# Optimization experiments

Measured on AMD Instinct MI355X. Metric: run time of the kernel, lower is better.

Reference implementation:

```python
import jax, jax.numpy as jnp
import numpy as np

SCALE_FACTORS = (0.5, 1.0)
ITERATIONS = (2, 2)
TAU = (1.0, 1.0)
SIGMA = (1.0, 1.0)
SIGMA_CUTOFF = 3.0
EPS = 1e-9
DHW = ('NCDHW', 'OIDHW', 'NCDHW')


def gaussian_kernel1d(sigma):
    radius = int(round(sigma * SIGMA_CUTOFF))
    x = np.arange(-radius, radius + 1, dtype=np.float32)
    k = np.exp(-0.5 * (x / sigma) ** 2)
    return jnp.asarray(k / k.sum())


def smooth3d(vf, kernel):
    # separable depthwise Gaussian over the 3 spatial axes; vf: (B,C,D,H,W)
    C = vf.shape[1]
    n = kernel.shape[0]
    for axis in range(3):
        shape = [1, 1, 1]
        shape[axis] = n
        kern = jnp.broadcast_to(kernel.reshape(1, 1, *shape), (C, 1, *shape))
        vf = jax.lax.conv_general_dilated(vf, kern, (1, 1, 1), 'SAME',
                                          feature_group_count=C, dimension_numbers=DHW)
    return vf


def resize_tri(x, spatial):
    return jax.image.resize(x, x.shape[:2] + tuple(spatial), method='trilinear')


def warp(img, flow):
    # trilinear grid-sample with voxel-space displacement, border clamping
    B, C, D, H, W = img.shape
    gz, gy, gx = jnp.meshgrid(jnp.arange(D, dtype=img.dtype),
                              jnp.arange(H, dtype=img.dtype),
                              jnp.arange(W, dtype=img.dtype), indexing='ij')
    base = jnp.stack([gz, gy, gx])  # (3,D,H,W)

    def one(im, fl):
        z = jnp.clip(base[0] + fl[0], 0.0, D - 1)
        y = jnp.clip(base[1] + fl[1], 0.0, H - 1)
        x = jnp.clip(base[2] + fl[2], 0.0, W - 1)
        z0 = jnp.floor(z); y0 = jnp.floor(y); x0 = jnp.floor(x)
        wz = z - z0; wy = y - y0; wx = x - x0
        z0i = z0.astype(jnp.int32); y0i = y0.astype(jnp.int32); x0i = x0.astype(jnp.int32)
        z1i = jnp.minimum(z0i + 1, D - 1)
        y1i = jnp.minimum(y0i + 1, H - 1)
        x1i = jnp.minimum(x0i + 1, W - 1)

        def g(zi, yi, xi):
            return im[:, zi, yi, xi]  # (C,D,H,W)

        return (g(z0i, y0i, x0i) * (1 - wz) * (1 - wy) * (1 - wx)
                + g(z0i, y0i, x1i) * (1 - wz) * (1 - wy) * wx
                + g(z0i, y1i, x0i) * (1 - wz) * wy * (1 - wx)
                + g(z0i, y1i, x1i) * (1 - wz) * wy * wx
                + g(z1i, y0i, x0i) * wz * (1 - wy) * (1 - wx)
                + g(z1i, y0i, x1i) * wz * (1 - wy) * wx
                + g(z1i, y1i, x0i) * wz * wy * (1 - wx)
                + g(z1i, y1i, x1i) * wz * wy * wx)

    return jax.vmap(one)(img, flow)


def demon_forces(warped, fixed):
    # 'active' demon forces: gradient of the warped moving image
    diff = warped - fixed                                  # (B,1,D,H,W)
    g = jnp.stack(jnp.gradient(warped[:, 0], axis=(1, 2, 3)), axis=1)  # (B,3,D,H,W)
    denom = jnp.sum(g * g, axis=1, keepdims=True) + diff * diff + EPS
    return diff * g / denom


def conv3(x, w, b=None):
    y = jax.lax.conv_general_dilated(x, w, (1, 1, 1), 'SAME', dimension_numbers=DHW)
    return y if b is None else y + b.reshape(1, -1, 1, 1, 1)


def inorm(x):  # InstanceNorm3d, affine=False, eps=1e-5
    m = x.mean(axis=(2, 3, 4), keepdims=True)
    v = x.var(axis=(2, 3, 4), keepdims=True)
    return (x - m) * jax.lax.rsqrt(v + 1e-5)


def mish(x):
    return x * jnp.tanh(jax.nn.softplus(x))


def updater(x, w1, w2, w3, w4, b4):
    x = mish(inorm(conv3(x, w1)))
    x = mish(inorm(conv3(x, w2)))
    x = mish(inorm(conv3(x, w3)))
    return conv3(x, w4, b4)


def match_vf(vf, spatial):
    old = vf.shape[2:]
    if tuple(old) == tuple(spatial):
        return vf
    vf2 = resize_tri(vf, spatial)
    scale = jnp.array([s1 / s2 for s1, s2 in zip(spatial, old)], dtype=vf.dtype)
    return vf2 * scale.reshape(1, 3, 1, 1, 1)


def registration(image, moving, w1, w2, w3, w4, b4):
    vf = None
    for i, (sf, iters) in enumerate(zip(SCALE_FACTORS, ITERATIONS)):
        spatial = tuple(int(s * sf) for s in image.shape[2:])
        si = resize_tri(image, spatial)
        smov = resize_tri(moving, spatial)
        vf = jnp.zeros((image.shape[0], 3) + spatial, image.dtype) if vf is None else match_vf(vf, spatial)
        kernel = gaussian_kernel1d(SIGMA[i]).astype(image.dtype)
        for _ in range(iters):
            warped = warp(smov, vf)
            forces = demon_forces(warped, si)
            feat = jnp.concatenate([forces, si, warped], axis=1)  # 5 channels
            vf = vf + TAU[i] * updater(feat, w1, w2, w3, w4, b4)
            vf = smooth3d(vf, kernel)
    vf = match_vf(vf, image.shape[2:])
    warped_full = warp(moving, vf)
    return warped_full, vf


def setup_inputs() -> dict:
    key = jax.random.key(0)
    ks = jax.random.split(key, 8)
    D = H = W = 96
    return {
        'image': jax.random.uniform(ks[0], (1, 1, D, H, W), jnp.float32),
        'mask': jnp.ones((1, 1, D, H, W), jnp.float32),
        'moving': jax.random.uniform(ks[1], (1, 1, D, H, W), jnp.float32),
        'spacing': jnp.ones((3,), jnp.float32),
        'w1': jax.random.normal(ks[2], (32, 5, 3, 3, 3), jnp.float32) * 0.05,
        'w2': jax.random.normal(ks[3], (64, 32, 3, 3, 3), jnp.float32) * 0.05,
        'w3': jax.random.normal(ks[4], (32, 64, 3, 3, 3), jnp.float32) * 0.05,
        'w4': jax.random.normal(ks[5], (3, 32, 3, 3, 3), jnp.float32) * 0.05,
        'b4': jnp.zeros((3,), jnp.float32),
    }


def reference(image, mask, moving, spacing, w1, w2, w3, w4, b4):
    # mask only feeds metrics/early-stopping (disabled: early_stopping_fn='none');
    # spacing unused since use_image_spacing=False.
    return registration(image, moving, w1, w2, w3, w4, b4)
```

## Files before the change

### kernel.cpp

```cpp
#include <hip/hip_runtime.h>
#include <hip/hip_bf16.h>


#define DEV __device__ __forceinline__
typedef __hip_bfloat16 bf16;
typedef __attribute__((ext_vector_type(8))) short short8;
typedef __attribute__((ext_vector_type(4))) float f32x4;

DEV float bfu(unsigned int u) {
  union { unsigned int i; float f; } x; x.i = u << 16; return x.f;
}
DEV unsigned short fbf(float f) {
  __hip_bfloat16 h = __float2bfloat16(f);
  return __builtin_bit_cast(unsigned short, h);
}

DEV float mishf(float v) {
  if (v > 20.f) return v;
  float u = __expf(v);
  float w = u * (u + 2.f);
  return v * (w / (w + 2.f));
}

__global__ void zero_k(float* __restrict__ p, int n) {
  int i = blockIdx.x * 256 + threadIdx.x;
  if (i < n) p[i] = 0.f;
}
__global__ void copy_k(const float* __restrict__ in, float* __restrict__ out, int n) {
  int i = blockIdx.x * 256 + threadIdx.x;
  if (i < n) out[i] = in[i];
}

__global__ void pack_wf_k(const float* __restrict__ w, bf16* __restrict__ dst,
                          int NWT, int KB, int COR, int CIR) {
  int idx = blockIdx.x * 256 + threadIdx.x;
  int tot = 27 * NWT * KB * 512;
  if (idx >= tot) return;
  int j = idx & 7;
  int lane = (idx >> 3) & 63;
  int frag = idx >> 9;
  int kb = frag % KB;
  int r2 = frag / KB;
  int nwt = r2 % NWT;
  int off = r2 / NWT;
  int co = nwt * 16 + (lane & 15);
  int ci = (kb * 4 + (lane >> 4)) * 8 + j;
  float v = (co < COR && ci < CIR) ? w[((size_t)co * CIR + ci) * 27 + off] : 0.f;
  dst[idx] = __float2bfloat16(v);
}

__global__ void pack_w1p_k(const float* __restrict__ w, bf16* __restrict__ dst) {
  int idx = blockIdx.x * 256 + threadIdx.x;
  if (idx >= 7 * 2 * 512) return;
  int j = idx & 7;
  int lane = (idx >> 3) & 63;
  int frag = idx >> 9;
  int nw = frag & 1;
  int rd = frag >> 1;
  int co = nw * 16 + (lane & 15);
  int tap = rd * 4 + (lane >> 4);
  float v = (tap < 27 && j < 5) ? w[((size_t)co * 5 + j) * 27 + tap] : 0.f;
  dst[idx] = __float2bfloat16(v);
}

DEV int ds_taps(int i, int n_out, int* j0, float* w) {
  if (i == 0) { *j0 = 0; w[0] = 3.f/7.f; w[1] = 3.f/7.f; w[2] = 1.f/7.f; return 3; }
  if (i == n_out - 1) { *j0 = 2*i - 1; w[0] = 1.f/7.f; w[1] = 3.f/7.f; w[2] = 3.f/7.f; return 3; }
  *j0 = 2*i - 1; w[0] = 0.125f; w[1] = 0.375f; w[2] = 0.375f; w[3] = 0.125f; return 4;
}
DEV void up_taps(int i, int n_in, int* j0, int* j1, float* w0, float* w1) {
  if (i & 1) {
    int k = i >> 1;
    if (k + 1 >= n_in) { *j0 = n_in - 1; *j1 = n_in - 1; *w0 = 1.f; *w1 = 0.f; }
    else { *j0 = k; *j1 = k + 1; *w0 = 0.75f; *w1 = 0.25f; }
  } else {
    int k = i >> 1;
    if (k == 0) { *j0 = 0; *j1 = 0; *w0 = 1.f; *w1 = 0.f; }
    else { *j0 = k - 1; *j1 = k; *w0 = 0.25f; *w1 = 0.75f; }
  }
}

__global__ void down2x_k(const float* __restrict__ in, float* __restrict__ out,
                         int Do, int Ho, int Wo) {
  const int Hi = 2 * Ho, Wi = 2 * Wo;
  const int No = Do * Ho * Wo;
  int i = blockIdx.x * 256 + threadIdx.x;
  if (i >= No) return;
  int xo = i % Wo; int t = i / Wo; int yo = t % Ho; int zo = t / Ho;
  int jz0, jy0, jx0; float wz[4], wy[4], wx[4];
  int cz = ds_taps(zo, Do, &jz0, wz);
  int cy = ds_taps(yo, Ho, &jy0, wy);
  int cx = ds_taps(xo, Wo, &jx0, wx);
  float s = 0.f;
  for (int a = 0; a < cz; ++a) {
    const float* pz = in + (size_t)(jz0 + a) * Hi * Wi;
    for (int b = 0; b < cy; ++b) {
      const float* py = pz + (size_t)(jy0 + b) * Wi;
      float wab = wz[a] * wy[b];
      for (int d = 0; d < cx; ++d) s += wab * wx[d] * py[jx0 + d];
    }
  }
  out[i] = s;
}

__global__ void up2x_vf_k(const float* __restrict__ in, float* __restrict__ out,
                          int Do, int Ho, int Wo) {
  const int Di = Do / 2, Hi = Ho / 2, Wi = Wo / 2;
  const int No = Do * Ho * Wo;
  const int c = blockIdx.y;
  int i = blockIdx.x * 256 + threadIdx.x;
  if (i >= No) return;
  int xo = i % Wo; int t = i / Wo; int yo = t % Ho; int zo = t / Ho;
  int jz0, jz1, jy0, jy1, jx0, jx1; float wz0, wz1, wy0, wy1, wx0, wx1;
  up_taps(zo, Di, &jz0, &jz1, &wz0, &wz1);
  up_taps(yo, Hi, &jy0, &jy1, &wy0, &wy1);
  up_taps(xo, Wi, &jx0, &jx1, &wx0, &wx1);
  const float* p = in + (size_t)c * Di * Hi * Wi;
  float v00 = wx0 * p[(jz0 * Hi + jy0) * Wi + jx0] + wx1 * p[(jz0 * Hi + jy0) * Wi + jx1];
  float v01 = wx0 * p[(jz0 * Hi + jy1) * Wi + jx0] + wx1 * p[(jz0 * Hi + jy1) * Wi + jx1];
  float v10 = wx0 * p[(jz1 * Hi + jy0) * Wi + jx0] + wx1 * p[(jz1 * Hi + jy0) * Wi + jx1];
  float v11 = wx0 * p[(jz1 * Hi + jy1) * Wi + jx0] + wx1 * p[(jz1 * Hi + jy1) * Wi + jx1];
  float s = wz0 * (wy0 * v00 + wy1 * v01) + wz1 * (wy0 * v10 + wy1 * v11);
  out[(size_t)c * No + i] = 2.f * s;
}

DEV float warp1(const float* __restrict__ img, const float* __restrict__ vf,
                int x, int y, int z, size_t i, int D, int H, int W, size_t N) {
  float zc = fminf(fmaxf((float)z + vf[i], 0.f), (float)(D - 1));
  float yc = fminf(fmaxf((float)y + vf[N + i], 0.f), (float)(H - 1));
  float xc = fminf(fmaxf((float)x + vf[2 * N + i], 0.f), (float)(W - 1));
  float zf = floorf(zc), yf = floorf(yc), xf = floorf(xc);
  int z0 = (int)zf, y0 = (int)yf, x0 = (int)xf;
  float wz = zc - zf, wy = yc - yf, wx = xc - xf;
  int z1 = min(z0 + 1, D - 1), y1 = min(y0 + 1, H - 1), x1 = min(x0 + 1, W - 1);
  const int HW = H * W;
  float v000 = img[z0 * HW + y0 * W + x0];
  float v001 = img[z0 * HW + y0 * W + x1];
  float v010 = img[z0 * HW + y1 * W + x0];
  float v011 = img[z0 * HW + y1 * W + x1];
  float v100 = img[z1 * HW + y0 * W + x0];
  float v101 = img[z1 * HW + y0 * W + x1];
  float v110 = img[z1 * HW + y1 * W + x0];
  float v111 = img[z1 * HW + y1 * W + x1];
  return v000 * (1 - wz) * (1 - wy) * (1 - wx)
       + v001 * (1 - wz) * (1 - wy) * wx
       + v010 * (1 - wz) * wy * (1 - wx)
       + v011 * (1 - wz) * wy * wx
       + v100 * wz * (1 - wy) * (1 - wx)
       + v101 * wz * (1 - wy) * wx
       + v110 * wz * wy * (1 - wx)
       + v111 * wz * wy * wx;
}

__global__ void warp_k(const float* __restrict__ img, const float* __restrict__ vf,
                       float* __restrict__ out, int D, int H, int W) {
  const size_t N = (size_t)D * H * W;
  size_t i = (size_t)blockIdx.x * 256 + threadIdx.x;
  if (i >= N) return;
  int x = i % W; int t = i / W; int y = t % H; int z = t / H;
  out[i] = warp1(img, vf, x, y, z, i, D, H, W, N);
}

__global__ void __launch_bounds__(256) warpforce_k(
    const float* __restrict__ img, const float* __restrict__ vf,
    const float* __restrict__ si, bf16* __restrict__ feat, int D, int H, int W) {
  __shared__ float wt[600];
  const size_t N = (size_t)D * H * W;
  const int t = threadIdx.x;
  const int tx = t & 7, ty = (t >> 3) & 7, tz = t >> 6;
  const int gx0 = blockIdx.x * 8, gy0 = blockIdx.y * 8, gz0 = blockIdx.z * 4;
  for (int cid = t; cid < 600; cid += 256) {
    int hx = cid % 10; int r = cid / 10; int hy = r % 10; int hz = r / 10;
    int gz = gz0 + hz - 1, gy = gy0 + hy - 1, gx = gx0 + hx - 1;
    float w = 0.f;
    if (((unsigned)gz < (unsigned)D) & ((unsigned)gy < (unsigned)H) & ((unsigned)gx < (unsigned)W)) {
      size_t i = (size_t)(gz * H + gy) * W + gx;
      w = warp1(img, vf, gx, gy, gz, i, D, H, W, N);
    }
    wt[cid] = w;
  }
  __syncthreads();
  const int x = gx0 + tx, y = gy0 + ty, z = gz0 + tz;
  const size_t i = (size_t)(z * H + y) * W + x;
  const int c = (tz + 1) * 100 + (ty + 1) * 10 + (tx + 1);
  float wv = wt[c];
  float gz = (z == 0) ? (wt[c + 100] - wv) : (z == D - 1) ? (wv - wt[c - 100]) : 0.5f * (wt[c + 100] - wt[c - 100]);
  float gy = (y == 0) ? (wt[c + 10] - wv) : (y == H - 1) ? (wv - wt[c - 10]) : 0.5f * (wt[c + 10] - wt[c - 10]);
  float gx = (x == 0) ? (wt[c + 1] - wv) : (x == W - 1) ? (wv - wt[c - 1]) : 0.5f * (wt[c + 1] - wt[c - 1]);
  float s = si[i];
  float diff = wv - s;
  float denom = gz * gz + gy * gy + gx * gx + diff * diff + 1e-9f;
  short8 o;
  o[0] = (short)fbf((diff * gz) / denom);
  o[1] = (short)fbf((diff * gy) / denom);
  o[2] = (short)fbf((diff * gx) / denom);
  o[3] = (short)fbf(s);
  o[4] = (short)fbf(wv);
  o[5] = 0; o[6] = 0; o[7] = 0;
  *(short8*)((short*)feat + i * 8) = o;
}

template <int TZ, int TY>
__global__ void __launch_bounds__(512) conv1p_k(
    const bf16* __restrict__ feat, const bf16* __restrict__ wpk,
    bf16* __restrict__ out, double* __restrict__ pbuf, int D, int H, int W) {
  constexpr int HZ = TZ + 2, HY = TY + 2;
  constexpr int HALO = HZ * HY * 18;
  constexpr int MS = TZ * TY / 4;
  __shared__ short lds[HALO * 8];
  __shared__ float2 red[8][1][16];
  const int t = threadIdx.x;
  const int gx0 = blockIdx.x * 16, gy0 = blockIdx.y * TY, gz0 = blockIdx.z * TZ;
  const short* featS = (const short*)feat;
  for (int pos = t; pos < HALO; pos += 512) {
    int hx = pos % 18; int r = pos / 18; int hy = r % HY; int hz = r / HY;
    int gz = gz0 + hz - 1, gy = gy0 + hy - 1, gx = gx0 + hx - 1;
    uint4 v = {0u, 0u, 0u, 0u};
    if (((unsigned)gz < (unsigned)D) & ((unsigned)gy < (unsigned)H) & ((unsigned)gx < (unsigned)W))
      v = *(const uint4*)(featS + ((size_t)(gz * H + gy) * W + gx) * 8);
    *(uint4*)(lds + pos * 8) = v;
  }
  __syncthreads();
  const int lane = t & 63, wid = t >> 6;
  const int mw = wid & 3, nw = wid >> 2;
  const int lid = lane & 15, kg = lane >> 4;
  f32x4 acc[MS];
#pragma unroll
  for (int ms = 0; ms < MS; ++ms) acc[ms] = {0.f, 0.f, 0.f, 0.f};
  int rowpos[MS];
#pragma unroll
  for (int ms = 0; ms < MS; ++ms) {
    int r = mw * MS + ms;
    rowpos[ms] = ((r / TY) * HY + (r % TY)) * 18 + lid;
  }
  const short* wp = (const short*)wpk;
#pragma unroll
  for (int rd = 0; rd < 7; ++rd) {
    int tap = rd * 4 + kg;
    int tp = tap > 26 ? 26 : tap;
    int kz = tp / 9, ky = (tp / 3) % 3, kx = tp % 3;
    int delta = (kz * HY + ky) * 18 + kx;
    short8 b = *(const short8*)(wp + ((size_t)(rd * 2 + nw) << 9) + lane * 8);
#pragma unroll
    for (int ms = 0; ms < MS; ++ms) {
      short8 a = *(const short8*)(lds + (rowpos[ms] + delta) * 8);
      acc[ms] = __builtin_amdgcn_mfma_f32_16x16x32_bf16(a, b, acc[ms], 0, 0, 0);
    }
  }
  const int xe = kg * 4;
#pragma unroll
  for (int ms = 0; ms < MS; ++ms) {
    int r = mw * MS + ms;
    int z = gz0 + r / TY, y = gy0 + r % TY;
    size_t voxb = (size_t)(z * H + y) * W + gx0;
    int co = nw * 16 + lid;
#pragma unroll
    for (int rg = 0; rg < 4; ++rg)
      out[(voxb + xe + rg) * 32 + co] = __float2bfloat16(acc[ms][rg]);
  }
  {
    float s = 0.f, q = 0.f;
#pragma unroll
    for (int ms = 0; ms < MS; ++ms)
#pragma unroll
      for (int rg = 0; rg < 4; ++rg) {
        float v = acc[ms][rg];
        s += v; q += v * v;
      }
    s += __shfl_xor(s, 16); q += __shfl_xor(q, 16);
    s += __shfl_xor(s, 32); q += __shfl_xor(q, 32);
    if (lane < 16) red[wid][0][lane] = make_float2(s, q);
    __syncthreads();
    if (t < 32) {
      const int nw_ = t >> 4, lid_ = t & 15;
      float S = 0.f, Q = 0.f;
#pragma unroll
      for (int m = 0; m < 4; ++m) {
        float2 v = red[nw_ * 4 + m][0][lid_];
        S += v.x; Q += v.y;
      }
      const int G = gridDim.x * gridDim.y * gridDim.z;
      const int bid = blockIdx.x + gridDim.x * (blockIdx.y + gridDim.y * blockIdx.z);
      pbuf[((size_t)t * G + bid) * 2 + 0] = (double)S;
      pbuf[((size_t)t * G + bid) * 2 + 1] = (double)Q;
    }
  }
}

template <int CIN, int COUT, int TZ, int TY, int INS, int REDUCE>
__global__ void __launch_bounds__(512) convmf_k(
    const bf16* __restrict__ act, const bf16* __restrict__ wpk,
    bf16* __restrict__ out, double* __restrict__ pbuf, int D, int H, int W) {
  constexpr int CH = CIN / 8;
  constexpr int RBS = CIN + 8;
  constexpr int HZ = TZ + 2, HY = TY + 2;
  constexpr int HALO = HZ * HY * 18;
  constexpr int MS = TZ * TY / 4;
  constexpr int NS = COUT / 32;
  constexpr int NWT = COUT / 16;
  constexpr int KB = CIN / 32;
  __shared__ short lds[HALO * RBS];
  __shared__ float2 red[8][NS][16];
  const int t = threadIdx.x;
  const int gx0 = blockIdx.x * 16, gy0 = blockIdx.y * TY, gz0 = blockIdx.z * TZ;
  const short* actS = (const short*)act;
  for (int cid = t; cid < HALO * CH; cid += 512) {
    int pos = cid / CH, c = cid - pos * CH;
    int hx = pos % 18; int r = pos / 18; int hy = r % HY; int hz = r / HY;
    int gz = gz0 + hz - 1, gy = gy0 + hy - 1, gx = gx0 + hx - 1;
    uint4 v = {0u, 0u, 0u, 0u};
    if (((unsigned)gz < (unsigned)D) & ((unsigned)gy < (unsigned)H) & ((unsigned)gx < (unsigned)W)) {
      size_t vox = (size_t)(gz * H + gy) * W + gx;
      if (INS == 8) { if (c == 0) v = *(const uint4*)(actS + vox * 8); }
      else v = *(const uint4*)(actS + vox * CIN + c * 8);
    }
    *(uint4*)(lds + pos * RBS + c * 8) = v;
  }
  __syncthreads();
  const int lane = t & 63, wid = t >> 6;
  const int mw = wid & 3, nw = wid >> 2;
  const int lid = lane & 15, kg = lane >> 4;
  f32x4 acc[MS][NS];
#pragma unroll
  for (int ms = 0; ms < MS; ++ms)
#pragma unroll
    for (int n = 0; n < NS; ++n) acc[ms][n] = {0.f, 0.f, 0.f, 0.f};
  int rowbase[MS];
#pragma unroll
  for (int ms = 0; ms < MS; ++ms) {
    int r = mw * MS + ms;
    rowbase[ms] = (((r / TY) * HY + (r % TY)) * 18 + lid) * RBS + kg * 8;
  }
  const short* wp = (const short*)wpk;
#pragma unroll 1
  for (int kz = 0; kz < 3; ++kz)
#pragma unroll 1
    for (int ky = 0; ky < 3; ++ky) {
      const int dbase = ((kz * HY + ky) * 18) * RBS;
#pragma unroll
      for (int kx = 0; kx < 3; ++kx) {
        const int off = (kz * 3 + ky) * 3 + kx;
        short8 bq[NS][KB];
#pragma unroll
        for (int n = 0; n < NS; ++n)
#pragma unroll
          for (int kb = 0; kb < KB; ++kb)
            bq[n][kb] = *(const short8*)(wp + ((((size_t)off * NWT + nw * NS + n) * KB + kb) << 9) + lane * 8);
#pragma unroll
        for (int ms = 0; ms < MS; ++ms) {
#pragma unroll
          for (int kb = 0; kb < KB; ++kb) {
            short8 a = *(const short8*)(lds + rowbase[ms] + dbase + kx * RBS + kb * 32);
#pragma unroll
            for (int n = 0; n < NS; ++n)
              acc[ms][n] = __builtin_amdgcn_mfma_f32_16x16x32_bf16(a, bq[n][kb], acc[ms][n], 0, 0, 0);
          }
        }
      }
    }
  const int xe = kg * 4;
#pragma unroll
  for (int ms = 0; ms < MS; ++ms) {
    int r = mw * MS + ms;
    int z = gz0 + r / TY, y = gy0 + r % TY;
    size_t voxb = (size_t)(z * H + y) * W + gx0;
#pragma unroll
    for (int n = 0; n < NS; ++n) {
      int co = nw * NS * 16 + n * 16 + lid;
#pragma unroll
      for (int rg = 0; rg < 4; ++rg)
        out[(voxb + xe + rg) * COUT + co] = __float2bfloat16(acc[ms][n][rg]);
    }
  }
  if (REDUCE) {
#pragma unroll
    for (int n = 0; n < NS; ++n) {
      float s = 0.f, q = 0.f;
#pragma unroll
      for (int ms = 0; ms < MS; ++ms)
#pragma unroll
        for (int rg = 0; rg < 4; ++rg) {
          float v = acc[ms][n][rg];
          s += v; q += v * v;
        }
      s += __shfl_xor(s, 16); q += __shfl_xor(q, 16);
      s += __shfl_xor(s, 32); q += __shfl_xor(q, 32);
      if (lane < 16) red[wid][n][lane] = make_float2(s, q);
    }
    __syncthreads();
    if (t < COUT) {
      const int nw_ = t / (NS * 16);
      const int rem = t - nw_ * NS * 16;
      const int n_ = rem >> 4, lid_ = rem & 15;
      float S = 0.f, Q = 0.f;
#pragma unroll
      for (int m = 0; m < 4; ++m) {
        float2 v = red[nw_ * 4 + m][n_][lid_];
        S += v.x; Q += v.y;
      }
      const int G = gridDim.x * gridDim.y * gridDim.z;
      const int bid = blockIdx.x + gridDim.x * (blockIdx.y + gridDim.y * blockIdx.z);
      pbuf[((size_t)t * G + bid) * 2 + 0] = (double)S;
      pbuf[((size_t)t * G + bid) * 2 + 1] = (double)Q;
    }
  }
}

template <int TZ, int TY>
__global__ void __launch_bounds__(512) conv4mf_k(
    const bf16* __restrict__ act, const bf16* __restrict__ wpk,
    const float* __restrict__ bias, float* __restrict__ vf, int D, int H, int W) {
  constexpr int CH = 4;
  constexpr int RBS = 40;
  constexpr int HZ = TZ + 2, HY = TY + 2;
  constexpr int HALO = HZ * HY * 18;
  constexpr int MS = TZ * TY / 8;
  __shared__ short lds[HALO * RBS];
  const int t = threadIdx.x;
  const int gx0 = blockIdx.x * 16, gy0 = blockIdx.y * TY, gz0 = blockIdx.z * TZ;
  const int N = D * H * W;
  const short* actS = (const short*)act;
  for (int cid = t; cid < HALO * CH; cid += 512) {
    int pos = cid / CH, c = cid - pos * CH;
    int hx = pos % 18; int r = pos / 18; int hy = r % HY; int hz = r / HY;
    int gz = gz0 + hz - 1, gy = gy0 + hy - 1, gx = gx0 + hx - 1;
    uint4 v = {0u, 0u, 0u, 0u};
    if (((unsigned)gz < (unsigned)D) & ((unsigned)gy < (unsigned)H) & ((unsigned)gx < (unsigned)W))
      v = *(const uint4*)(actS + ((size_t)(gz * H + gy) * W + gx) * 32 + c * 8);
    *(uint4*)(lds + pos * RBS + c * 8) = v;
  }
  __syncthreads();
  const int lane = t & 63, wid = t >> 6;
  const int lid = lane & 15, kg = lane >> 4;
  f32x4 acc[MS];
#pragma unroll
  for (int ms = 0; ms < MS; ++ms) acc[ms] = {0.f, 0.f, 0.f, 0.f};
  int rowbase[MS];
#pragma unroll
  for (int ms = 0; ms < MS; ++ms) {
    int r = wid * MS + ms;
    rowbase[ms] = (((r / TY) * HY + (r % TY)) * 18 + lid) * RBS + kg * 8;
  }
  const short* wp = (const short*)wpk;
#pragma unroll 1
  for (int kz = 0; kz < 3; ++kz)
#pragma unroll 1
    for (int ky = 0; ky < 3; ++ky) {
      const int dbase = ((kz * HY + ky) * 18) * RBS;
#pragma unroll
      for (int kx = 0; kx < 3; ++kx) {
        const int off = (kz * 3 + ky) * 3 + kx;
        short8 b = *(const short8*)(wp + ((size_t)off << 9) + lane * 8);
#pragma unroll
        for (int ms = 0; ms < MS; ++ms) {
          short8 a = *(const short8*)(lds + rowbase[ms] + dbase + kx * RBS);
          acc[ms] = __builtin_amdgcn_mfma_f32_16x16x32_bf16(a, b, acc[ms], 0, 0, 0);
        }
      }
    }
  if (lid < 3) {
    float bs = bias[lid];
#pragma unroll
    for (int ms = 0; ms < MS; ++ms) {
      int r = wid * MS + ms;
      int z = gz0 + r / TY, y = gy0 + r % TY;
      size_t voxb = (size_t)(z * H + y) * W + gx0 + kg * 4;
      float* p = vf + (size_t)lid * N + voxb;
#pragma unroll
      for (int rg = 0; rg < 4; ++rg) p[rg] += acc[ms][rg] + bs;
    }
  }
}

__global__ void stage2_k(const double* __restrict__ pbuf, float2* __restrict__ musc,
                         int N, int G) {
  const int c = blockIdx.x;
  double S = 0, Q = 0;
  for (int g = threadIdx.x; g < G; g += 256) {
    S += pbuf[((size_t)c * G + g) * 2 + 0];
    Q += pbuf[((size_t)c * G + g) * 2 + 1];
  }
  for (int off = 32; off > 0; off >>= 1) {
    S += __shfl_down(S, off); Q += __shfl_down(Q, off);
  }
  __shared__ double ls[4], lq[4];
  const int wid = threadIdx.x >> 6, lane = threadIdx.x & 63;
  if (lane == 0) { ls[wid] = S; lq[wid] = Q; }
  __syncthreads();
  if (threadIdx.x == 0) {
    double St = ls[0] + ls[1] + ls[2] + ls[3];
    double Qt = lq[0] + lq[1] + lq[2] + lq[3];
    double m = St / N;
    double var = Qt / N - m * m;
    musc[c] = make_float2((float)m, (float)(1.0 / sqrt(var + 1e-5)));
  }
}

template <int C>
__global__ void inorm_vc_k(bf16* __restrict__ x, const float2* __restrict__ musc, int N) {
  constexpr int CP = C / 2;
  constexpr int VPB = 256 / CP;
  const int cp = threadIdx.x & (CP - 1);
  const int vt = threadIdx.x / CP;
  float2 m0 = musc[2 * cp], m1 = musc[2 * cp + 1];
  unsigned int* p = (unsigned int*)x;
  int v0 = blockIdx.x * (4 * VPB) + vt;
#pragma unroll
  for (int r = 0; r < 4; ++r) {
    int v = v0 + r * VPB;
    size_t idx = (size_t)v * CP + cp;
    unsigned int u = p[idx];
    float a = mishf((bfu(u & 0xffffu) - m0.x) * m0.y);
    float b = mishf((bfu(u >> 16) - m1.x) * m1.y);
    p[idx] = (unsigned int)fbf(a) | ((unsigned int)fbf(b) << 16);
  }
}

template <int AXIS>
__global__ void smooth_k(const float* __restrict__ in, float* __restrict__ out,
                         int D, int H, int W) {
  const int N = D * H * W;
  const int c = blockIdx.y;
  int i = blockIdx.x * 256 + threadIdx.x;
  if (i >= N) return;
  int x = i % W; int t = i / W; int y = t % H; int z = t / H;
  const int coord = AXIS == 0 ? z : AXIS == 1 ? y : x;
  const int len = AXIS == 0 ? D : AXIS == 1 ? H : W;
  const int stride = AXIS == 0 ? H * W : AXIS == 1 ? W : 1;
  const float k1 = 0.60653065971263342f, k2 = 0.13533528323661270f, k3 = 0.011108996538242306f;
  const float kn = 1.f / (1.f + 2.f * (k1 + k2 + k3));
  const float gw[4] = {kn, k1 * kn, k2 * kn, k3 * kn};
  const float* p = in + (size_t)c * N;
  float s = gw[0] * p[i];
#pragma unroll
  for (int tt = 1; tt <= 3; ++tt) {
    if (coord - tt >= 0) s += gw[tt] * p[i - tt * stride];
    if (coord + tt < len) s += gw[tt] * p[i + tt * stride];
  }
  out[(size_t)c * N + i] = s;
}

extern "C" void kernel_launch(void* const* d_in, const int* in_sizes, int n_in,
                              void* d_out, int out_size, void* d_ws, size_t ws_size,
                              hipStream_t stream) {
  const float* image  = (const float*)d_in[0];
  const float* moving = (const float*)d_in[2];
  const float* w1 = (const float*)d_in[4];
  const float* w2 = (const float*)d_in[5];
  const float* w3 = (const float*)d_in[6];
  const float* w4 = (const float*)d_in[7];
  const float* b4 = (const float*)d_in[8];
  float* out = (float*)d_out;

  const int D1 = 96; const int N1 = D1 * D1 * D1;
  const int D0 = 48; const int N0 = D0 * D0 * D0;

  char* wsp = (char*)d_ws;
  double* pbuf  = (double*)wsp;          wsp += (size_t)64 * 13824 * 2 * 8;
  float2* musc  = (float2*)wsp;          wsp += 1024;
  bf16* w1p     = (bf16*)wsp;            wsp += 27 * 2 * 1 * 512 * 2;
  bf16* w2p     = (bf16*)wsp;            wsp += 27 * 4 * 1 * 512 * 2;
  bf16* w3p     = (bf16*)wsp;            wsp += 27 * 2 * 2 * 512 * 2;
  bf16* w4p     = (bf16*)wsp;            wsp += 27 * 1 * 1 * 512 * 2;
  float* si0    = (float*)wsp;           wsp += (size_t)N0 * 4;
  float* smov0  = (float*)wsp;           wsp += (size_t)N0 * 4;
  float* vf0    = (float*)wsp;           wsp += 3 * (size_t)N1 * 4;
  float* vf1    = (float*)wsp;           wsp += 3 * (size_t)N1 * 4;
  bf16* feat    = (bf16*)wsp;            wsp += 8 * (size_t)N1 * 2;
  bf16* bufA    = (bf16*)wsp;            wsp += 32 * (size_t)N1 * 2;
  bf16* bufB    = (bf16*)wsp;            wsp += 64 * (size_t)N1 * 2;

  pack_w1p_k<<<(7 * 2 * 512 + 255) / 256, 256, 0, stream>>>(w1, w1p);
  pack_wf_k<<<(27 * 4 * 512 + 255) / 256, 256, 0, stream>>>(w2, w2p, 4, 1, 64, 32);
  pack_wf_k<<<(27 * 4 * 512 + 255) / 256, 256, 0, stream>>>(w3, w3p, 2, 2, 32, 64);
  pack_wf_k<<<(27 * 1 * 512 + 255) / 256, 256, 0, stream>>>(w4, w4p, 1, 1, 3, 32);

  down2x_k<<<N0 / 256, 256, 0, stream>>>(image, si0, D0, D0, D0);
  down2x_k<<<N0 / 256, 256, 0, stream>>>(moving, smov0, D0, D0, D0);
  zero_k<<<3 * N0 / 256, 256, 0, stream>>>(vf0, 3 * N0);

  float* vfc = vf0;
  float* vfa = vf1;

  auto run_level = [&](const float* si, const float* smov, int Dd) {
    const int N = Dd * Dd * Dd;
    const int nb = N / 256;
    const dim3 gw(Dd / 8, Dd / 8, Dd / 4);
    const dim3 g1(Dd / 16, Dd / 4, Dd / 4);
    const dim3 g3(Dd / 16, Dd / 4, Dd / 2);
    const int G1 = g1.x * g1.y * g1.z;
    const int G3 = g3.x * g3.y * g3.z;
    for (int it = 0; it < 2; ++it) {
      warpforce_k<<<gw, 256, 0, stream>>>(smov, vfc, si, feat, Dd, Dd, Dd);

      conv1p_k<4, 4><<<g1, 512, 0, stream>>>(feat, w1p, bufA, pbuf, Dd, Dd, Dd);
      stage2_k<<<32, 256, 0, stream>>>(pbuf, musc, N, G1);
      inorm_vc_k<32><<<N / 64, 256, 0, stream>>>(bufA, musc, N);

      convmf_k<32, 64, 4, 4, 32, 1><<<g1, 512, 0, stream>>>(bufA, w2p, bufB, pbuf, Dd, Dd, Dd);
      stage2_k<<<64, 256, 0, stream>>>(pbuf, musc, N, G1);
      inorm_vc_k<64><<<N / 32, 256, 0, stream>>>(bufB, musc, N);

      convmf_k<64, 32, 2, 4, 64, 1><<<g3, 512, 0, stream>>>(bufB, w3p, bufA, pbuf, Dd, Dd, Dd);
      stage2_k<<<32, 256, 0, stream>>>(pbuf, musc, N, G3);
      inorm_vc_k<32><<<N / 64, 256, 0, stream>>>(bufA, musc, N);

      conv4mf_k<4, 4><<<g1, 512, 0, stream>>>(bufA, w4p, b4, vfc, Dd, Dd, Dd);

      smooth_k<0><<<dim3(nb, 3), 256, 0, stream>>>(vfc, vfa, Dd, Dd, Dd);
      smooth_k<1><<<dim3(nb, 3), 256, 0, stream>>>(vfa, vfc, Dd, Dd, Dd);
      smooth_k<2><<<dim3(nb, 3), 256, 0, stream>>>(vfc, vfa, Dd, Dd, Dd);
      { float* tmp = vfc; vfc = vfa; vfa = tmp; }
    }
  };

  run_level(si0, smov0, D0);

  up2x_vf_k<<<dim3(N1 / 256, 3), 256, 0, stream>>>(vfc, vfa, D1, D1, D1);
  { float* tmp = vfc; vfc = vfa; vfa = tmp; }

  run_level(image, moving, D1);

  warp_k<<<N1 / 256, 256, 0, stream>>>(moving, vfc, out, D1, D1, D1);
  copy_k<<<3 * N1 / 256, 256, 0, stream>>>(vfc, out + N1, 3 * N1);
}
```

Measured before the change: 1.257 ms.

## Fuse separable 3D smoothing into one tiled shared-memory kernel and drop final copy

Replaces three per-axis Gaussian smoothing launches with a single kernel that loads a haloed 14^3 tile into shared memory and applies the z, y, x passes in LDS. The last smoothing pass at full resolution writes directly into the output buffer, removing the trailing copy kernel. This cuts global memory round-trips and launches, at the cost of redundant halo loads and more shared memory per block.

```diff
diff --git a/kernel.cpp b/kernel.cpp
--- a/kernel.cpp
+++ b/kernel.cpp
@@ -25,10 +25,6 @@
 __global__ void zero_k(float* __restrict__ p, int n) {
   int i = blockIdx.x * 256 + threadIdx.x;
   if (i < n) p[i] = 0.f;
-}
-__global__ void copy_k(const float* __restrict__ in, float* __restrict__ out, int n) {
-  int i = blockIdx.x * 256 + threadIdx.x;
-  if (i < n) out[i] = in[i];
 }
 
 __global__ void pack_wf_k(const float* __restrict__ w, bf16* __restrict__ dst,
@@ -516,28 +512,61 @@
   }
 }
 
-template <int AXIS>
-__global__ void smooth_k(const float* __restrict__ in, float* __restrict__ out,
-                         int D, int H, int W) {
-  const int N = D * H * W;
-  const int c = blockIdx.y;
-  int i = blockIdx.x * 256 + threadIdx.x;
-  if (i >= N) return;
-  int x = i % W; int t = i / W; int y = t % H; int z = t / H;
-  const int coord = AXIS == 0 ? z : AXIS == 1 ? y : x;
-  const int len = AXIS == 0 ? D : AXIS == 1 ? H : W;
-  const int stride = AXIS == 0 ? H * W : AXIS == 1 ? W : 1;
+__global__ void __launch_bounds__(256) smooth3_k(
+    const float* __restrict__ in, float* __restrict__ outp, int D, int H, int W) {
+  __shared__ float a[14 * 14 * 14];
+  __shared__ float b[8 * 14 * 14];
+  __shared__ float c2[8 * 8 * 14];
+  const int t = threadIdx.x;
+  const int ztiles = D / 8;
+  const int ch = blockIdx.z / ztiles;
+  const int zt = blockIdx.z % ztiles;
+  const int gx0 = blockIdx.x * 8 - 3, gy0 = blockIdx.y * 8 - 3, gz0 = zt * 8 - 3;
+  const size_t Nv = (size_t)D * H * W;
+  const float* p = in + (size_t)ch * Nv;
   const float k1 = 0.60653065971263342f, k2 = 0.13533528323661270f, k3 = 0.011108996538242306f;
   const float kn = 1.f / (1.f + 2.f * (k1 + k2 + k3));
-  const float gw[4] = {kn, k1 * kn, k2 * kn, k3 * kn};
-  const float* p = in + (size_t)c * N;
-  float s = gw[0] * p[i];
-#pragma unroll
-  for (int tt = 1; tt <= 3; ++tt) {
-    if (coord - tt >= 0) s += gw[tt] * p[i - tt * stride];
-    if (coord + tt < len) s += gw[tt] * p[i + tt * stride];
-  }
-  out[(size_t)c * N + i] = s;
+  const float g0 = kn, g1 = k1 * kn, g2 = k2 * kn, g3 = k3 * kn;
+  for (int cid = t; cid < 14 * 14 * 14; cid += 256) {
+    int xx = cid % 14; int r = cid / 14; int yy = r % 14; int zz = r / 14;
+    int gz = gz0 + zz, gy = gy0 + yy, gx = gx0 + xx;
+    float v = 0.f;
+    if (((unsigned)gz < (unsigned)D) & ((unsigned)gy < (unsigned)H) & ((unsigned)gx < (unsigned)W))
+      v = p[(size_t)(gz * H + gy) * W + gx];
+    a[cid] = v;
+  }
+  __syncthreads();
+  for (int cid = t; cid < 8 * 14 * 14; cid += 256) {
+    int xx = cid % 14; int r = cid / 14; int yy = r % 14; int zz = r / 14;
+    int base = ((zz + 3) * 14 + yy) * 14 + xx;
+    float s = g0 * a[base];
+    s += g1 * a[base - 196]; s += g1 * a[base + 196];
+    s += g2 * a[base - 392]; s += g2 * a[base + 392];
+    s += g3 * a[base - 588]; s += g3 * a[base + 588];
+    b[cid] = s;
+  }
+  __syncthreads();
+  for (int cid = t; cid < 8 * 8 * 14; cid += 256) {
+    int xx = cid % 14; int r = cid / 14; int yy = r % 8; int zz = r / 8;
+    int base = (zz * 14 + yy + 3) * 14 + xx;
+    float s = g0 * b[base];
+    s += g1 * b[base - 14]; s += g1 * b[base + 14];
+    s += g2 * b[base - 28]; s += g2 * b[base + 28];
+    s += g3 * b[base - 42]; s += g3 * b[base + 42];
+    c2[cid] = s;
+  }
+  __syncthreads();
+  float* q = outp + (size_t)ch * Nv;
+  for (int cid = t; cid < 8 * 8 * 8; cid += 256) {
+    int xx = cid & 7; int r = cid >> 3; int yy = r & 7; int zz = r >> 3;
+    int base = (zz * 8 + yy) * 14 + xx + 3;
+    float s = g0 * c2[base];
+    s += g1 * c2[base - 1]; s += g1 * c2[base + 1];
+    s += g2 * c2[base - 2]; s += g2 * c2[base + 2];
+    s += g3 * c2[base - 3]; s += g3 * c2[base + 3];
+    int gz = gz0 + 3 + zz, gy = gy0 + 3 + yy, gx = gx0 + 3 + xx;
+    q[(size_t)(gz * H + gy) * W + gx] = s;
+  }
 }
 
 extern "C" void kernel_launch(void* const* d_in, const int* in_sizes, int n_in,
@@ -582,12 +611,12 @@
   float* vfc = vf0;
   float* vfa = vf1;
 
-  auto run_level = [&](const float* si, const float* smov, int Dd) {
+  auto run_level = [&](const float* si, const float* smov, int Dd, float* last_dst) {
     const int N = Dd * Dd * Dd;
-    const int nb = N / 256;
     const dim3 gw(Dd / 8, Dd / 8, Dd / 4);
     const dim3 g1(Dd / 16, Dd / 4, Dd / 4);
     const dim3 g3(Dd / 16, Dd / 4, Dd / 2);
+    const dim3 gs(Dd / 8, Dd / 8, (Dd / 8) * 3);
     const int G1 = g1.x * g1.y * g1.z;
     const int G3 = g3.x * g3.y * g3.z;
     for (int it = 0; it < 2; ++it) {
@@ -607,20 +636,18 @@
 
       conv4mf_k<4, 4><<<g1, 512, 0, stream>>>(bufA, w4p, b4, vfc, Dd, Dd, Dd);
 
-      smooth_k<0><<<dim3(nb, 3), 256, 0, stream>>>(vfc, vfa, Dd, Dd, Dd);
-      smooth_k<1><<<dim3(nb, 3), 256, 0, stream>>>(vfa, vfc, Dd, Dd, Dd);
-      smooth_k<2><<<dim3(nb, 3), 256, 0, stream>>>(vfc, vfa, Dd, Dd, Dd);
-      { float* tmp = vfc; vfc = vfa; vfa = tmp; }
+      float* dst = (it == 1 && last_dst) ? last_dst : vfa;
+      smooth3_k<<<gs, 256, 0, stream>>>(vfc, dst, Dd, Dd, Dd);
+      vfa = vfc; vfc = dst;
     }
   };
 
-  run_level(si0, smov0, D0);
+  run_level(si0, smov0, D0, nullptr);
 
   up2x_vf_k<<<dim3(N1 / 256, 3), 256, 0, stream>>>(vfc, vfa, D1, D1, D1);
   { float* tmp = vfc; vfc = vfa; vfa = tmp; }
 
-  run_level(image, moving, D1);
+  run_level(image, moving, D1, out + N1);
 
   warp_k<<<N1 / 256, 256, 0, stream>>>(moving, vfc, out, D1, D1, D1);
-  copy_k<<<3 * N1 / 256, 256, 0, stream>>>(vfc, out + N1, 3 * N1);
-}
+}
```

Result: faster. 1.206 ms (-4.1%).
